# Performance work log

Hardware: AMD Instinct MI355X
Metric: run time of the kernel (lower is better)

## Reference

```python
import jax, jax.numpy as jnp
import numpy as np

TEMPERATURE = 0.5
SCALE_BY_TEMPERATURE = True
CURV = 0.05

N = 8192
D = 128
N_PRIMARY = 32
N_SECONDARY = 16


def setup_inputs() -> dict:
    key = jax.random.key(0)
    k1, k2, k3 = jax.random.split(key, 3)
    features = jax.random.normal(k1, (N, D), dtype=jnp.float32)
    primary_labels = jax.random.randint(k2, (N,), 0, N_PRIMARY)
    secondary_labels = jax.random.randint(k3, (N,), 0, N_SECONDARY)
    return {"features": features, "primary_labels": primary_labels,
            "secondary_labels": secondary_labels}


def _hyp_contrastive_loss(features, primary_labels, secondary_labels):
    c = CURV
    sqrt_c = c ** 0.5
    n = features.shape[0]

    # L2 normalize (torch F.normalize with eps=1e-12)
    nrm = jnp.maximum(jnp.linalg.norm(features, axis=1, keepdims=True), 1e-12)
    f = features / nrm

    # Pairwise mobius_add(-f[j], f[i]) at [i, j]. With x = -f[j], y = f[i]:
    #   num = (1 + 2c<x,y> + c|y|^2) x + (1 - c|x|^2) y,   den = 1 + 2c<x,y> + c^2|x|^2|y|^2
    # We only need ||num||/den, so expand ||num||^2 algebraically to avoid an
    # [N, N, D] intermediate (same math, exact).
    n2 = jnp.sum(f * f, axis=1)            # [N], ~1 after normalize
    s = f @ f.T                            # [N, N] <f_i, f_j>
    xy = -s                                # <x, y>
    x2 = n2[None, :]                       # |x|^2 = |f_j|^2
    y2 = n2[:, None]                       # |y|^2 = |f_i|^2

    A = 1.0 + 2.0 * c * xy + c * y2
    B = 1.0 - c * x2
    den = jnp.maximum(1.0 + 2.0 * c * xy + c * c * x2 * y2, 1e-15)
    num_sq = jnp.maximum(A * A * x2 + 2.0 * A * B * xy + B * B * y2, 0.0)
    norm_diff = sqrt_c * jnp.sqrt(num_sq) / den           # [N, N]

    # artanh with clamp (pm.artanh clamps argument below 1)
    distance = jnp.arctanh(jnp.clip(norm_diff, 0.0, 1.0 - 1e-7)) * 2.0 / sqrt_c

    anchor_dot_contrast = -distance / TEMPERATURE
    logits_max = jax.lax.stop_gradient(
        jnp.max(anchor_dot_contrast, axis=1, keepdims=True))
    logits = anchor_dot_contrast - logits_max
    exp_logits = jnp.exp(logits)

    pmask = (primary_labels[:, None] == primary_labels[None, :]).astype(f.dtype)
    smask = (secondary_labels[:, None] == secondary_labels[None, :]).astype(f.dtype)
    combined = jnp.minimum(pmask + smask, 1.0)

    eye = jnp.eye(n, dtype=f.dtype)
    positives_mask = combined * (1.0 - eye)
    negatives_mask = 1.0 - combined

    num_pos = jnp.sum(positives_mask, axis=1)             # [N]
    valid = num_pos > 0

    pos_contrib = jnp.sum(exp_logits * positives_mask, axis=1)
    neg_contrib = jnp.sum(exp_logits * negatives_mask, axis=1)
    denominator = pos_contrib + neg_contrib + 1e-8        # [N]

    log_probs = logits - jnp.log(denominator)[:, None]
    row_sum = jnp.sum(log_probs * positives_mask, axis=1)
    per_row = jnp.where(valid, row_sum / jnp.maximum(num_pos, 1.0), 0.0)

    n_valid = jnp.sum(valid.astype(f.dtype))
    loss = -jnp.sum(per_row) / jnp.maximum(n_valid, 1.0)  # mean over valid rows
    loss = jnp.where(n_valid > 0, loss, 0.0)
    if SCALE_BY_TEMPERATURE:
        loss = loss * TEMPERATURE
    return jnp.nan_to_num(loss, nan=0.0, posinf=0.0, neginf=0.0)


def reference(features, primary_labels, secondary_labels):
    return _hyp_contrastive_loss(features, primary_labels, secondary_labels)
```

## Files before the change

kernel.cpp:

```cpp
#include <hip/hip_runtime.h>
#include <hip/hip_bf16.h>

#define NN 8192
#define DD 128

typedef short short8 __attribute__((ext_vector_type(8)));
typedef __bf16 bf16x8 __attribute__((ext_vector_type(8)));
typedef float f32x4 __attribute__((ext_vector_type(4)));
typedef float f32x2 __attribute__((ext_vector_type(2)));

#define MKc (-0.110803324099723f)
#define PKc (0.110803324099723f)
#define C1Kc (1.110803324099723f)
#define KEc (-8.944271909999159f)
#define KLc (-6.199696797323639f)

__global__ __launch_bounds__(256) void prep_kernel(const float* __restrict__ x,
                                                   __hip_bfloat16* __restrict__ fb,
                                                   float* __restrict__ totg,
                                                   float* __restrict__ tposg,
                                                   float* __restrict__ scal,
                                                   int* __restrict__ dcnt) {
  int r = threadIdx.x >> 4, sub = threadIdx.x & 15;
  int row = blockIdx.x * 16 + r;
  const float4 a = *(const float4*)(x + (size_t)row * DD + sub * 8);
  const float4 b = *(const float4*)(x + (size_t)row * DD + sub * 8 + 4);
  float ss = a.x * a.x + a.y * a.y + a.z * a.z + a.w * a.w +
             b.x * b.x + b.y * b.y + b.z * b.z + b.w * b.w;
  for (int off = 1; off < 16; off <<= 1) ss += __shfl_xor(ss, off, 16);
  float inv = 1.0f / fmaxf(sqrtf(ss), 1e-12f);
  float va[8] = {a.x, a.y, a.z, a.w, b.x, b.y, b.z, b.w};
  short8 h;
  for (int j = 0; j < 8; j++) {
    __hip_bfloat16 t = __float2bfloat16(va[j] * inv);
    h[j] = __builtin_bit_cast(short, t);
  }
  *(short8*)((short*)fb + (size_t)row * DD + sub * 8) = h;
  if (threadIdx.x < 16) {
    totg[blockIdx.x * 16 + threadIdx.x] = 0.f;
    tposg[blockIdx.x * 16 + threadIdx.x] = 0.f;
  } else if (blockIdx.x == 0 && threadIdx.x < 20) {
    if (threadIdx.x == 16) scal[0] = 0.f;
    if (threadIdx.x == 17) scal[1] = 0.f;
    if (threadIdx.x == 18) dcnt[0] = 0;
    if (threadIdx.x == 19) dcnt[1] = 0;
  }
}

__global__ __launch_bounds__(256, 2) void fused_kernel(
    const __hip_bfloat16* __restrict__ fbg,
    const int* __restrict__ plab, const int* __restrict__ slab,
    float* __restrict__ totg, float* __restrict__ tposg) {
  __shared__ float colT_l[4 * 272];
  __shared__ float colG_l[4 * 272];

  const int tid = threadIdx.x;
  const int w = tid >> 6;
  const int lane = tid & 63;
  const int lrow = lane & 15;
  const int quad = lane >> 4;

  const int u = blockIdx.x >> 5;
  const int k = blockIdx.x & 31;
  const int s = (k < 8) ? 17 * k : 16 * k + 8;
  const int c = (k < 8) ? 17 : 16;
  const int B = 8 * (u + 1);

  const int aEnd = min(s + c, B);
  const int aCnt = max(0, aEnd - s);
  const int bStart = max(s, B);
  const int bCnt = max(0, s + c - bStart);
  int segR0[2], segCol[2], segCnt[2], segLds[2];
  segR0[0] = 128 * u;        segCol[0] = s * 16;              segCnt[0] = aCnt; segLds[0] = 0;
  segR0[1] = 128 * (63 - u); segCol[1] = (bStart - B) * 16;   segCnt[1] = bCnt; segLds[1] = aCnt;

  for (int i = lane; i < 272; i += 64) {
    colT_l[w * 272 + i] = 0.f;
    colG_l[w * 272 + i] = 0.f;
  }

  const f32x2 MK2 = {MKc, MKc}, PK2 = {PKc, PKc}, C1K2 = {C1Kc, C1Kc};
  const f32x2 KE2 = {KEc, KEc}, ZERO2 = {0.f, 0.f}, TWO2 = {2.f, 2.f};

  for (int seg = 0; seg < 2; seg++) {
    const int cnt = segCnt[seg];
    if (cnt == 0) continue;
    const int R0 = segR0[seg];
    const int colBase = segCol[seg];
    const int ldsBase = segLds[seg];

    bf16x8 af[2][4];
    int plr[2][4], slr[2][4];
    for (int strip = 0; strip < 2; strip++) {
      const short* fa = (const short*)fbg + (size_t)(R0 + w * 32 + strip * 16 + lrow) * DD;
      for (int kk = 0; kk < 4; kk++)
        af[strip][kk] = __builtin_bit_cast(bf16x8, *(const short8*)(fa + kk * 32 + quad * 8));
      for (int r = 0; r < 4; r++) {
        int rowg = R0 + w * 32 + strip * 16 + quad * 4 + r;
        plr[strip][r] = plab[rowg];
        slr[strip][r] = slab[rowg];
      }
    }

    f32x2 t2[2][2], g2[2][2];
    for (int s_ = 0; s_ < 2; s_++)
      for (int p = 0; p < 2; p++) { t2[s_][p] = ZERO2; g2[s_][p] = ZERO2; }

    const short* bp = (const short*)fbg + (size_t)(colBase + lrow) * DD + quad * 8;
    int colg = colBase + lrow;

    for (int ct = 0; ct < cnt; ct++) {
      bf16x8 bf[4];
      for (int kk = 0; kk < 4; kk++)
        bf[kk] = __builtin_bit_cast(bf16x8, *(const short8*)(bp + kk * 32));
      bp += 16 * DD;

      f32x4 acc[2];
      for (int strip = 0; strip < 2; strip++) {
        f32x4 a0 = {0.f, 0.f, 0.f, 0.f};
        for (int kk = 0; kk < 4; kk++)
          a0 = __builtin_amdgcn_mfma_f32_16x16x32_bf16(af[strip][kk], bf[kk], a0, 0, 0, 0);
        acc[strip] = a0;
      }

      const int pc = plab[colg];
      const int sc = slab[colg];
      const bool mct = (colg - lrow + 240 >= R0);
      f32x2 colE = ZERO2, colL = ZERO2;

      for (int strip = 0; strip < 2; strip++) {
        for (int p = 0; p < 2; p++) {
          f32x2 s2 = {acc[strip][2 * p], acc[strip][2 * p + 1]};
          f32x2 tK = __builtin_elementwise_fma(s2, MK2, PK2);
          tK = __builtin_elementwise_max(tK, ZERO2);
          f32x2 dk = __builtin_elementwise_fma(s2, MK2, C1K2);
          f32x2 m = tK * dk;
          f32x2 sq = {__builtin_amdgcn_sqrtf(m.x), __builtin_amdgcn_sqrtf(m.y)};
          f32x2 tpd = tK + dk;
          f32x2 rr = __builtin_elementwise_fma(sq, TWO2, tpd);
          f32x2 lg = {__log2f(rr.x), __log2f(rr.y)};
          f32x2 el = KE2 * lg;
          f32x2 e = {exp2f(el.x), exp2f(el.y)};
          const int r0 = 2 * p, r1 = 2 * p + 1;
          bool same0 = (pc == plr[strip][r0]) || (sc == slr[strip][r0]);
          bool same1 = (pc == plr[strip][r1]) || (sc == slr[strip][r1]);
          f32x2 em, lm;
          if (mct) {
            int rg0 = R0 + w * 32 + strip * 16 + quad * 4 + r0;
            bool ok0 = (colg < rg0);
            bool ok1 = (colg < rg0 + 1);
            em.x = ok0 ? e.x : 0.f;
            em.y = ok1 ? e.y : 0.f;
            lm.x = (same0 && ok0) ? lg.x : 0.f;
            lm.y = (same1 && ok1) ? lg.y : 0.f;
          } else {
            em = e;
            lm.x = same0 ? lg.x : 0.f;
            lm.y = same1 ? lg.y : 0.f;
          }
          t2[strip][p] += em;
          g2[strip][p] += lm;
          colE += em;
          colL += lm;
        }
      }

      float cE = colE.x + colE.y;
      float cL = colL.x + colL.y;
      cE += __shfl_xor(cE, 16, 64);
      cE += __shfl_xor(cE, 32, 64);
      cL += __shfl_xor(cL, 16, 64);
      cL += __shfl_xor(cL, 32, 64);
      if (quad == 0) {
        colT_l[w * 272 + (ldsBase + ct) * 16 + lrow] += cE;
        colG_l[w * 272 + (ldsBase + ct) * 16 + lrow] += cL;
      }
      colg += 16;
    }

    for (int strip = 0; strip < 2; strip++) {
      for (int r = 0; r < 4; r++) {
        float t = t2[strip][r >> 1][r & 1];
        float g = g2[strip][r >> 1][r & 1];
        for (int off = 1; off < 16; off <<= 1) {
          t += __shfl_xor(t, off, 16);
          g += __shfl_xor(g, off, 16);
        }
        if (lrow == 0) {
          int rowg = R0 + w * 32 + strip * 16 + quad * 4 + r;
          atomicAdd(&totg[rowg], t);
          atomicAdd(&tposg[rowg], g);
        }
      }
    }
  }

  __syncthreads();
  const int total = (aCnt + bCnt) * 16;
  for (int i = tid; i < total; i += 256) {
    const int ct = i >> 4;
    const int cin = i & 15;
    int col;
    if (ct < aCnt) col = segCol[0] + (ct - segLds[0]) * 16 + cin;
    else col = segCol[1] + (ct - segLds[1]) * 16 + cin;
    float sE = colT_l[i] + colT_l[272 + i] + colT_l[544 + i] + colT_l[816 + i];
    float sL = colG_l[i] + colG_l[272 + i] + colG_l[544 + i] + colG_l[816 + i];
    atomicAdd(&totg[col], sE);
    atomicAdd(&tposg[col], sL);
  }
}

__global__ __launch_bounds__(256) void finalize_k(const float* __restrict__ totg,
                                                  const float* __restrict__ tposg,
                                                  const int* __restrict__ plab,
                                                  const int* __restrict__ slab,
                                                  float* __restrict__ scal,
                                                  int* __restrict__ dcnt,
                                                  float* __restrict__ out) {
  __shared__ int hist[512];
  __shared__ int cntP[32], cntS[16];
  __shared__ float redP[4], redV[4];
  const int tid = threadIdx.x;
  hist[tid] = 0;
  hist[tid + 256] = 0;
  __syncthreads();
  for (int i = tid; i < NN; i += 256)
    atomicAdd(&hist[plab[i] * 16 + slab[i]], 1);
  __syncthreads();
  if (tid < 32) {
    int s = 0;
    for (int j = 0; j < 16; j++) s += hist[tid * 16 + j];
    cntP[tid] = s;
  } else if (tid < 48) {
    int s = 0;
    for (int j = 0; j < 32; j++) s += hist[j * 16 + (tid - 32)];
    cntS[tid - 32] = s;
  }
  __syncthreads();
  const int row = blockIdx.x * 256 + tid;
  const int pl = plab[row], sl = slab[row];
  const int np = cntP[pl] + cntS[sl] - hist[pl * 16 + sl] - 1;
  float accP = 0.f, accV = 0.f;
  if (np > 0) {
    accP = (KLc * tposg[row]) / (float)np - __logf(totg[row] + 1e-8f);
    accV = 1.f;
  }
  for (int off = 32; off; off >>= 1) {
    accP += __shfl_xor(accP, off, 64);
    accV += __shfl_xor(accV, off, 64);
  }
  if ((tid & 63) == 0) { redP[tid >> 6] = accP; redV[tid >> 6] = accV; }
  __syncthreads();
  if (tid == 0) {
    atomicAdd(&scal[0], redP[0] + redP[1] + redP[2] + redP[3]);
    atomicAdd(&scal[1], redV[0] + redV[1] + redV[2] + redV[3]);
    __threadfence();
    if (atomicAdd(dcnt, 1) == 31) {
      const float sp = __hip_atomic_load(&scal[0], __ATOMIC_ACQUIRE,
                                         __HIP_MEMORY_SCOPE_AGENT);
      const float sv = __hip_atomic_load(&scal[1], __ATOMIC_ACQUIRE,
                                         __HIP_MEMORY_SCOPE_AGENT);
      float loss = -(sp / fmaxf(sv, 1.0f)) * 0.5f;
      if (sv <= 0.0f || !__builtin_isfinite(loss)) loss = 0.0f;
      out[0] = loss;
    }
  }
}

extern "C" void kernel_launch(void* const* d_in, const int* in_sizes, int n_in,
                              void* d_out, int out_size, void* d_ws, size_t ws_size,
                              hipStream_t stream) {
  const float* x = (const float*)d_in[0];
  const int* pl = (const int*)d_in[1];
  const int* sl = (const int*)d_in[2];
  char* ws = (char*)d_ws;
  __hip_bfloat16* fb = (__hip_bfloat16*)ws;
  float* totg = (float*)(ws + 2097152);
  float* tposg = (float*)(ws + 2129920);
  float* scal = (float*)(ws + 2162688);
  int* dcnt = (int*)(ws + 2162696);

  prep_kernel<<<NN / 16, 256, 0, stream>>>(x, fb, totg, tposg, scal, dcnt);
  fused_kernel<<<1024, 256, 0, stream>>>(fb, pl, sl, totg, tposg);
  finalize_k<<<32, 256, 0, stream>>>(totg, tposg, pl, sl, scal, dcnt, (float*)d_out);
}
```

Before: 112.0 us.

## Prefetch next column tile's B fragments and labels; use LDS atomics for column sums

Software-pipelines the column loop: the B-operand bf16 fragments and column labels for the next tile are loaded while the current tile's MFMA and transcendental math run, hiding global load latency. It also replaces the cross-quad shuffle reduction of the per-column sums with direct LDS atomicAdd from every lane. The prefetch raises register pressure. The LDS atomics add contention across the four quads, and the summation order changes.

```diff
diff --git a/kernel.cpp b/kernel.cpp
--- a/kernel.cpp
+++ b/kernel.cpp
@@ -109,22 +109,28 @@
     const short* bp = (const short*)fbg + (size_t)(colBase + lrow) * DD + quad * 8;
     int colg = colBase + lrow;
 
+    bf16x8 bfc[4];
+    for (int kk = 0; kk < 4; kk++)
+      bfc[kk] = __builtin_bit_cast(bf16x8, *(const short8*)(bp + kk * 32));
+    int pcc = plab[colg], scc = slab[colg];
+
     for (int ct = 0; ct < cnt; ct++) {
-      bf16x8 bf[4];
+      const bool more = (ct + 1 < cnt);
+      const short* bpn = bp + (more ? 16 * DD : 0);
+      const int colgn = more ? colg + 16 : colg;
+      bf16x8 bfn[4];
       for (int kk = 0; kk < 4; kk++)
-        bf[kk] = __builtin_bit_cast(bf16x8, *(const short8*)(bp + kk * 32));
-      bp += 16 * DD;
+        bfn[kk] = __builtin_bit_cast(bf16x8, *(const short8*)(bpn + kk * 32));
+      const int pcn = plab[colgn], scn = slab[colgn];
 
       f32x4 acc[2];
       for (int strip = 0; strip < 2; strip++) {
         f32x4 a0 = {0.f, 0.f, 0.f, 0.f};
         for (int kk = 0; kk < 4; kk++)
-          a0 = __builtin_amdgcn_mfma_f32_16x16x32_bf16(af[strip][kk], bf[kk], a0, 0, 0, 0);
+          a0 = __builtin_amdgcn_mfma_f32_16x16x32_bf16(af[strip][kk], bfc[kk], a0, 0, 0, 0);
         acc[strip] = a0;
       }
 
-      const int pc = plab[colg];
-      const int sc = slab[colg];
       const bool mct = (colg - lrow + 240 >= R0);
       f32x2 colE = ZERO2, colL = ZERO2;
 
@@ -142,8 +148,8 @@
           f32x2 el = KE2 * lg;
           f32x2 e = {exp2f(el.x), exp2f(el.y)};
           const int r0 = 2 * p, r1 = 2 * p + 1;
-          bool same0 = (pc == plr[strip][r0]) || (sc == slr[strip][r0]);
-          bool same1 = (pc == plr[strip][r1]) || (sc == slr[strip][r1]);
+          bool same0 = (pcc == plr[strip][r0]) || (scc == slr[strip][r0]);
+          bool same1 = (pcc == plr[strip][r1]) || (scc == slr[strip][r1]);
           f32x2 em, lm;
           if (mct) {
             int rg0 = R0 + w * 32 + strip * 16 + quad * 4 + r0;
@@ -165,16 +171,12 @@
         }
       }
 
-      float cE = colE.x + colE.y;
-      float cL = colL.x + colL.y;
-      cE += __shfl_xor(cE, 16, 64);
-      cE += __shfl_xor(cE, 32, 64);
-      cL += __shfl_xor(cL, 16, 64);
-      cL += __shfl_xor(cL, 32, 64);
-      if (quad == 0) {
-        colT_l[w * 272 + (ldsBase + ct) * 16 + lrow] += cE;
-        colG_l[w * 272 + (ldsBase + ct) * 16 + lrow] += cL;
-      }
+      atomicAdd(&colT_l[w * 272 + (ldsBase + ct) * 16 + lrow], colE.x + colE.y);
+      atomicAdd(&colG_l[w * 272 + (ldsBase + ct) * 16 + lrow], colL.x + colL.y);
+
+      for (int kk = 0; kk < 4; kk++) bfc[kk] = bfn[kk];
+      pcc = pcn; scc = scn;
+      bp += 16 * DD;
       colg += 16;
     }
 
```

After: 135.1 us. +20.6%, slower.

## Double-buffer B tiles via global_load_lds and use LDS atomics for column sums

Applied to the files above, without the earlier changes.

Column-tile B fragments are now prefetched one iteration ahead straight into LDS with global_load_lds, into a per-wave double buffer, so the global load latency overlaps the MFMA and epilogue work. The per-wave column partial arrays are merged into a single shared array that is updated with LDS atomicAdd. This removes the cross-quad shuffles and the final four-way sum. The trade-offs are LDS atomic contention across lanes and waves, plus a full vmcnt(0) wait at the top of every iteration.

```diff
diff --git a/kernel.cpp b/kernel.cpp
--- a/kernel.cpp
+++ b/kernel.cpp
@@ -8,6 +8,9 @@
 typedef __bf16 bf16x8 __attribute__((ext_vector_type(8)));
 typedef float f32x4 __attribute__((ext_vector_type(4)));
 typedef float f32x2 __attribute__((ext_vector_type(2)));
+
+#define AS1 __attribute__((address_space(1)))
+#define AS3 __attribute__((address_space(3)))
 
 #define MKc (-0.110803324099723f)
 #define PKc (0.110803324099723f)
@@ -51,8 +54,9 @@
     const __hip_bfloat16* __restrict__ fbg,
     const int* __restrict__ plab, const int* __restrict__ slab,
     float* __restrict__ totg, float* __restrict__ tposg) {
-  __shared__ float colT_l[4 * 272];
-  __shared__ float colG_l[4 * 272];
+  __shared__ short8 sB[4][2][4][64];
+  __shared__ float colT_l[272];
+  __shared__ float colG_l[272];
 
   const int tid = threadIdx.x;
   const int w = tid >> 6;
@@ -74,10 +78,11 @@
   segR0[0] = 128 * u;        segCol[0] = s * 16;              segCnt[0] = aCnt; segLds[0] = 0;
   segR0[1] = 128 * (63 - u); segCol[1] = (bStart - B) * 16;   segCnt[1] = bCnt; segLds[1] = aCnt;
 
-  for (int i = lane; i < 272; i += 64) {
-    colT_l[w * 272 + i] = 0.f;
-    colG_l[w * 272 + i] = 0.f;
-  }
+  for (int i = tid; i < 272; i += 256) {
+    colT_l[i] = 0.f;
+    colG_l[i] = 0.f;
+  }
+  __syncthreads();
 
   const f32x2 MK2 = {MKc, MKc}, PK2 = {PKc, PKc}, C1K2 = {C1Kc, C1Kc};
   const f32x2 KE2 = {KEc, KEc}, ZERO2 = {0.f, 0.f}, TWO2 = {2.f, 2.f};
@@ -106,14 +111,26 @@
     for (int s_ = 0; s_ < 2; s_++)
       for (int p = 0; p < 2; p++) { t2[s_][p] = ZERO2; g2[s_][p] = ZERO2; }
 
-    const short* bp = (const short*)fbg + (size_t)(colBase + lrow) * DD + quad * 8;
+    const short* gB = (const short*)fbg + (size_t)(colBase + lrow) * DD + quad * 8;
     int colg = colBase + lrow;
 
+    for (int kk = 0; kk < 4; kk++)
+      __builtin_amdgcn_global_load_lds((const AS1 void*)(gB + kk * 32),
+                                       (AS3 void*)&sB[w][0][kk][0], 16, 0, 0);
+    int cur = 0;
+
     for (int ct = 0; ct < cnt; ct++) {
+      asm volatile("s_waitcnt vmcnt(0)" ::: "memory");
+      if (ct + 1 < cnt) {
+        const short* gN = gB + 16 * DD;
+        for (int kk = 0; kk < 4; kk++)
+          __builtin_amdgcn_global_load_lds((const AS1 void*)(gN + kk * 32),
+                                           (AS3 void*)&sB[w][cur ^ 1][kk][0], 16, 0, 0);
+      }
+
       bf16x8 bf[4];
       for (int kk = 0; kk < 4; kk++)
-        bf[kk] = __builtin_bit_cast(bf16x8, *(const short8*)(bp + kk * 32));
-      bp += 16 * DD;
+        bf[kk] = __builtin_bit_cast(bf16x8, sB[w][cur][kk][lane]);
 
       f32x4 acc[2];
       for (int strip = 0; strip < 2; strip++) {
@@ -165,17 +182,12 @@
         }
       }
 
-      float cE = colE.x + colE.y;
-      float cL = colL.x + colL.y;
-      cE += __shfl_xor(cE, 16, 64);
-      cE += __shfl_xor(cE, 32, 64);
-      cL += __shfl_xor(cL, 16, 64);
-      cL += __shfl_xor(cL, 32, 64);
-      if (quad == 0) {
-        colT_l[w * 272 + (ldsBase + ct) * 16 + lrow] += cE;
-        colG_l[w * 272 + (ldsBase + ct) * 16 + lrow] += cL;
-      }
+      atomicAdd(&colT_l[(ldsBase + ct) * 16 + lrow], colE.x + colE.y);
+      atomicAdd(&colG_l[(ldsBase + ct) * 16 + lrow], colL.x + colL.y);
+
+      gB += 16 * DD;
       colg += 16;
+      cur ^= 1;
     }
 
     for (int strip = 0; strip < 2; strip++) {
@@ -203,10 +215,8 @@
     int col;
     if (ct < aCnt) col = segCol[0] + (ct - segLds[0]) * 16 + cin;
     else col = segCol[1] + (ct - segLds[1]) * 16 + cin;
-    float sE = colT_l[i] + colT_l[272 + i] + colT_l[544 + i] + colT_l[816 + i];
-    float sL = colG_l[i] + colG_l[272 + i] + colG_l[544 + i] + colG_l[816 + i];
-    atomicAdd(&totg[col], sE);
-    atomicAdd(&tposg[col], sL);
+    atomicAdd(&totg[col], colT_l[i]);
+    atomicAdd(&tposg[col], colG_l[i]);
   }
 }
 
```

New measurement: 132.5 us. 18.3% more time.
